# Kernel optimization log

Hardware: AMD Instinct MI355X
Metric: run time of the kernel (lower is better)

The kernel has to match this reference:

```python
import jax, jax.numpy as jnp
import numpy as np

N, CI, CO, K = 16384, 64, 64, 257


def setup_inputs() -> dict:
    key = jax.random.key(0)
    k1, k2 = jax.random.split(key)
    x = jax.random.normal(k1, (N, CI), dtype=jnp.float32)
    # lecun_normal-like scale over fan_in = K*CI
    kernel = jax.random.normal(k2, (K, CI, CO), dtype=jnp.float32) * (1.0 / np.sqrt(K * CI))
    bias = jnp.zeros((CO,), dtype=jnp.float32)
    return {"x": x, "kernel": kernel, "bias": bias}


def reference(x, kernel, bias):
    # Faithful translation of fconv1d.__call__ with strides=1, padding='valid'.
    Ci = x.shape[-1]
    Co = kernel.shape[-1]
    # h: (K, Ci*Co), flattened row-major so column j -> (ci=j//Co, co=j%Co)
    h = jnp.reshape(kernel, (kernel.shape[0], Ci * Co))
    # y: (N, Ci*Co), tiled so column j -> ci = j % Ci (exactly as jnp.tile does)
    y = jnp.tile(x, (1, Co))
    # Ci*Co independent 1D 'valid' convolutions (true convolution, kernel flipped)
    zflat = jax.vmap(lambda a, b: jnp.convolve(a, b, mode='valid'),
                     in_axes=-1, out_axes=-1)(y, h)  # (Nout, Ci*Co)
    # reduce over Ci exactly as the original reshape/sum does
    z = zflat.T.reshape((Co, Ci, -1)).sum(axis=1).T  # (Nout, Co)
    sps = 1  # strides = 1
    return z[::sps, :] + bias[None, :]
```

## Files before the change

### kernel.cpp

```cpp
#include <hip/hip_runtime.h>

#define NN   16384
#define CIN  64
#define COUT 64
#define KW   257
#define NOUT (NN - KW + 1)
#define BM   256
#define NKCH 8

typedef __attribute__((ext_vector_type(8))) short short8;
typedef __attribute__((ext_vector_type(8))) unsigned short ushortx8;
typedef __attribute__((ext_vector_type(4))) float floatx4;
typedef unsigned short ushort_t;

__device__ __forceinline__ ushort_t f2bf(float f) {
  union { float f; unsigned u; } c; c.f = f;
  unsigned u = c.u;
  return (ushort_t)((u + 0x7FFFu + ((u >> 16) & 1u)) >> 16);
}
__device__ __forceinline__ float bf2f(ushort_t h) {
  union { unsigned u; float f; } c; c.u = ((unsigned)h) << 16;
  return c.f;
}

__device__ __forceinline__ void cp16(const void* g, void* l) {
  auto gp = (const __attribute__((address_space(1))) unsigned int*)(unsigned long long)(uintptr_t)g;
  auto lp = (__attribute__((address_space(3))) unsigned int*)(unsigned int)(uintptr_t)l;
  __builtin_amdgcn_global_load_lds(gp, lp, 16, 0, 0);
}

__global__ void prep_convert(const float* __restrict__ x, const float* __restrict__ w,
                             ushort_t* __restrict__ xs, ushort_t* __restrict__ wsz) {
  const int c = blockIdx.x * blockDim.x + threadIdx.x;
  const float* src;
  ushort_t* dst;
  if (c < 131072) {
    const int row = c >> 3, ch = c & 7;
    src = x + (size_t)row * 64 + ((ch ^ (row & 7)) << 3);
    dst = xs + (size_t)row * 64 + (ch << 3);
  } else {
    const int c2 = c - 131072;
    const int t = c2 >> 9, r = (c2 >> 3) & 63, ch = c2 & 7;
    src = w + (size_t)(256 - t) * 4096 + r * 64 + ((ch ^ (r & 7)) << 3);
    dst = wsz + (size_t)t * 4096 + r * 64 + (ch << 3);
  }
  float4 v0 = *(const float4*)src;
  float4 v1 = *(const float4*)(src + 4);
  ushortx8 o;
  o[0] = f2bf(v0.x); o[1] = f2bf(v0.y); o[2] = f2bf(v0.z); o[3] = f2bf(v0.w);
  o[4] = f2bf(v1.x); o[5] = f2bf(v1.y); o[6] = f2bf(v1.z); o[7] = f2bf(v1.w);
  *(ushortx8*)dst = o;
}

__global__ __launch_bounds__(256, 2) void conv_gemm(
    const ushort_t* __restrict__ xs, const ushort_t* __restrict__ wsz,
    ushort_t* __restrict__ part) {
  __shared__ __align__(128) char smem[288 * 128 + 2 * 16384];
  char* Alds = smem;
  char* Wlds = smem + 288 * 128;

  const int tid  = threadIdx.x;
  const int lane = tid & 63;
  const int w    = tid >> 6;
  const int lr   = lane & 15;
  const int lh   = lane >> 4;

  const int mblk = blockIdx.x;
  const int g    = blockIdx.y;
  const int n0   = mblk * BM;
  const int t0   = (g * KW) / NKCH;
  const int t1   = ((g + 1) * KW) / NKCH;
  const int Tc   = t1 - t0;
  const int NCf  = Tc >> 1;
  const bool odd = Tc & 1;

  const ushort_t* agbase = xs + (size_t)(n0 + t0) * 64;
#pragma unroll
  for (int i = 0; i < 9; ++i)
    cp16(agbase + ((w * 9 + i) << 9) + lane * 8, Alds + ((w * 9 + i) << 10));

  const ushort_t* wgbase = wsz + (size_t)t0 * 4096;
#pragma unroll
  for (int s = 0; s < 2; ++s)
#pragma unroll
    for (int i = 0; i < 2; ++i)
      cp16(wgbase + (size_t)s * 4096 + ((w * 2 + i) << 9) + lane * 8,
           Wlds + s * 8192 + (w * 2 + i) * 1024);
  __syncthreads();

  floatx4 acc[4][4];
#pragma unroll
  for (int m = 0; m < 4; ++m)
#pragma unroll
    for (int nb = 0; nb < 4; ++nb)
      acc[m][nb] = (floatx4){0.f, 0.f, 0.f, 0.f};

  auto phase = [&](int ttL, int kk, const char* Wl) {
    short8 a[4], b[4];
#pragma unroll
    for (int m = 0; m < 4; ++m) {
      const int row = ttL + w * 64 + m * 16 + lr;
      a[m] = *(const short8*)(Alds + row * 128 + (((lh + 4 * kk) ^ (row & 7)) << 4));
    }
#pragma unroll
    for (int nb = 0; nb < 4; ++nb) {
      const int rw = nb * 16 + lr;
      b[nb] = *(const short8*)(Wl + rw * 128 + (((lh + 4 * kk) ^ (rw & 7)) << 4));
    }
    __builtin_amdgcn_s_barrier();
    asm volatile("s_waitcnt lgkmcnt(0)" ::: "memory");
    __builtin_amdgcn_sched_barrier(0);
    __builtin_amdgcn_s_setprio(1);
#pragma unroll
    for (int m = 0; m < 4; ++m)
#pragma unroll
      for (int nb = 0; nb < 4; ++nb)
        acc[m][nb] = __builtin_amdgcn_mfma_f32_16x16x32_bf16(a[m], b[nb], acc[m][nb], 0, 0, 0);
    __builtin_amdgcn_s_setprio(0);
    __builtin_amdgcn_s_barrier();
  };

  for (int cc = 0; cc < NCf; ++cc) {
    const int buf = cc & 1;
    if (cc + 1 < NCf) {
      const ushort_t* wg = wsz + (size_t)(t0 + (cc + 1) * 2) * 4096;
#pragma unroll
      for (int s = 0; s < 2; ++s)
#pragma unroll
        for (int i = 0; i < 2; ++i)
          cp16(wg + (size_t)s * 4096 + ((w * 2 + i) << 9) + lane * 8,
               Wlds + (buf ^ 1) * 16384 + s * 8192 + (w * 2 + i) * 1024);
      asm volatile("s_waitcnt vmcnt(4)" ::: "memory");
    } else if (odd) {
      const ushort_t* wg = wsz + (size_t)(t0 + NCf * 2) * 4096;
#pragma unroll
      for (int i = 0; i < 2; ++i)
        cp16(wg + ((w * 2 + i) << 9) + lane * 8,
             Wlds + (buf ^ 1) * 16384 + (w * 2 + i) * 1024);
      asm volatile("s_waitcnt vmcnt(2)" ::: "memory");
    } else {
      asm volatile("s_waitcnt vmcnt(0)" ::: "memory");
    }
    __builtin_amdgcn_s_barrier();

    const char* Wl = Wlds + buf * 16384;
    phase(cc * 2,     0, Wl);
    phase(cc * 2,     1, Wl);
    phase(cc * 2 + 1, 0, Wl + 8192);
    phase(cc * 2 + 1, 1, Wl + 8192);
  }
  if (odd) {
    asm volatile("s_waitcnt vmcnt(0)" ::: "memory");
    __builtin_amdgcn_s_barrier();
    const char* Wl = Wlds + (NCf & 1) * 16384;
    phase(Tc - 1, 0, Wl);
    phase(Tc - 1, 1, Wl);
  }

  ushort_t* pg = part + (size_t)g * (NOUT * 64);
#pragma unroll
  for (int m = 0; m < 4; ++m)
#pragma unroll
    for (int nb = 0; nb < 4; ++nb)
#pragma unroll
      for (int r = 0; r < 4; ++r) {
        const int row = n0 + w * 64 + m * 16 + lh * 4 + r;
        const int col = nb * 16 + lr;
        pg[(size_t)row * 64 + col] = f2bf(acc[m][nb][r]);
      }
}

__global__ void reduce_out(const ushort_t* __restrict__ part, const float* __restrict__ bias,
                           float* __restrict__ out) {
  const int i = blockIdx.x * blockDim.x + threadIdx.x;
  if (i >= NOUT * 8) return;
  const int colbase = (i & 7) * 8;
  float s[8];
#pragma unroll
  for (int j = 0; j < 8; ++j) s[j] = bias[colbase + j];
#pragma unroll
  for (int gg = 0; gg < NKCH; ++gg) {
    ushortx8 p = *(const ushortx8*)(part + (size_t)gg * (NOUT * 64) + (size_t)i * 8);
#pragma unroll
    for (int j = 0; j < 8; ++j) s[j] += bf2f(p[j]);
  }
  float4 o0 = {s[0], s[1], s[2], s[3]};
  float4 o1 = {s[4], s[5], s[6], s[7]};
  *(float4*)(out + (size_t)i * 8) = o0;
  *(float4*)(out + (size_t)i * 8 + 4) = o1;
}

__global__ void naive_conv(const float* __restrict__ x, const float* __restrict__ w,
                           const float* __restrict__ bias, float* __restrict__ out) {
  const int idx = blockIdx.x * blockDim.x + threadIdx.x;
  if (idx >= NOUT * COUT) return;
  const int n = idx / COUT, co = idx % COUT;
  float s = bias[co];
  for (int t = 0; t < KW; ++t) {
    const float* xr = x + (size_t)(n + t) * CIN;
    const float* wr = w + (size_t)(KW - 1 - t) * CIN * COUT + (size_t)co * CIN;
#pragma unroll 8
    for (int ci = 0; ci < CIN; ++ci) s += xr[ci] * wr[ci];
  }
  out[idx] = s;
}

extern "C" void kernel_launch(void* const* d_in, const int* in_sizes, int n_in,
                              void* d_out, int out_size, void* d_ws, size_t ws_size,
                              hipStream_t stream) {
  const float* x    = (const float*)d_in[0];
  const float* kern = (const float*)d_in[1];
  const float* bias = (const float*)d_in[2];
  float* out = (float*)d_out;

  const size_t xs_b   = (size_t)NN * CIN * 2;
  const size_t ws_b   = (size_t)KW * CIN * COUT * 2;
  const size_t part_b = (size_t)NKCH * NOUT * COUT * 2;
  const size_t need   = xs_b + ws_b + part_b;

  if (ws_size < need) {
    naive_conv<<<(NOUT * COUT + 255) / 256, 256, 0, stream>>>(x, kern, bias, out);
    return;
  }

  ushort_t* xs   = (ushort_t*)d_ws;
  ushort_t* wsz  = xs + (size_t)NN * CIN;
  ushort_t* part = wsz + (size_t)KW * CIN * COUT;

  prep_convert<<<1026, 256, 0, stream>>>(x, kern, xs, wsz);
  conv_gemm<<<dim3(NOUT / BM, NKCH), 256, 0, stream>>>(xs, wsz, part);
  reduce_out<<<(NOUT * 8 + 255) / 256, 256, 0, stream>>>(part, bias, out);
}
```

Baseline: 45.45 us.

## Double the M tile to 512 rows and pipeline weights one tap at a time

The conv GEMM block grows from 256 to 512 output rows with 512 threads, so each weight tap loaded into LDS is shared by twice as many rows. The old two-tap double buffer becomes a four-slot ring that prefetches one tap three steps ahead. The input is zero-padded so the last, partial tile can read past the end safely, and stores are masked for rows past the output length. The larger LDS footprint probably limits occupancy to one block per CU. Half of the last tile's compute is also wasted.

Result: slower. 47.84 us (+5.3%).

```diff
diff --git a/kernel.cpp b/kernel.cpp
--- a/kernel.cpp
+++ b/kernel.cpp
@@ -1,11 +1,12 @@
 #include <hip/hip_runtime.h>
 
 #define NN   16384
+#define NPAD 512
 #define CIN  64
 #define COUT 64
 #define KW   257
 #define NOUT (NN - KW + 1)
-#define BM   256
+#define BM   512
 #define NKCH 8
 
 typedef __attribute__((ext_vector_type(8))) short short8;
@@ -32,6 +33,12 @@
 __global__ void prep_convert(const float* __restrict__ x, const float* __restrict__ w,
                              ushort_t* __restrict__ xs, ushort_t* __restrict__ wsz) {
   const int c = blockIdx.x * blockDim.x + threadIdx.x;
+  if (c >= 262656) {
+    const int cz = c - 262656;
+    const int row = NN + (cz >> 3), ch = cz & 7;
+    *(ushortx8*)(xs + (size_t)row * 64 + (ch << 3)) = (ushortx8)(0);
+    return;
+  }
   const float* src;
   ushort_t* dst;
   if (c < 131072) {
@@ -52,12 +59,12 @@
   *(ushortx8*)dst = o;
 }
 
-__global__ __launch_bounds__(256, 2) void conv_gemm(
+__global__ __launch_bounds__(512, 2) void conv_gemm(
     const ushort_t* __restrict__ xs, const ushort_t* __restrict__ wsz,
     ushort_t* __restrict__ part) {
-  __shared__ __align__(128) char smem[288 * 128 + 2 * 16384];
+  __shared__ __align__(128) char smem[576 * 128 + 4 * 8192];
   char* Alds = smem;
-  char* Wlds = smem + 288 * 128;
+  char* Wlds = smem + 576 * 128;
 
   const int tid  = threadIdx.x;
   const int lane = tid & 63;
@@ -71,8 +78,6 @@
   const int t0   = (g * KW) / NKCH;
   const int t1   = ((g + 1) * KW) / NKCH;
   const int Tc   = t1 - t0;
-  const int NCf  = Tc >> 1;
-  const bool odd = Tc & 1;
 
   const ushort_t* agbase = xs + (size_t)(n0 + t0) * 64;
 #pragma unroll
@@ -81,12 +86,11 @@
 
   const ushort_t* wgbase = wsz + (size_t)t0 * 4096;
 #pragma unroll
-  for (int s = 0; s < 2; ++s)
-#pragma unroll
-    for (int i = 0; i < 2; ++i)
-      cp16(wgbase + (size_t)s * 4096 + ((w * 2 + i) << 9) + lane * 8,
-           Wlds + s * 8192 + (w * 2 + i) * 1024);
-  __syncthreads();
+  for (int t = 0; t < 3; ++t)
+    cp16(wgbase + (size_t)t * 4096 + (w << 9) + lane * 8,
+         Wlds + t * 8192 + (w << 10));
+  asm volatile("s_waitcnt vmcnt(2)" ::: "memory");
+  __builtin_amdgcn_s_barrier();
 
   floatx4 acc[4][4];
 #pragma unroll
@@ -95,66 +99,66 @@
     for (int nb = 0; nb < 4; ++nb)
       acc[m][nb] = (floatx4){0.f, 0.f, 0.f, 0.f};
 
-  auto phase = [&](int ttL, int kk, const char* Wl) {
-    short8 a[4], b[4];
-#pragma unroll
-    for (int m = 0; m < 4; ++m) {
-      const int row = ttL + w * 64 + m * 16 + lr;
-      a[m] = *(const short8*)(Alds + row * 128 + (((lh + 4 * kk) ^ (row & 7)) << 4));
+  for (int t = 0; t < Tc; ++t) {
+    const char* Wt = Wlds + (t & 3) * 8192;
+    {
+      short8 a[4], b[4];
+#pragma unroll
+      for (int m = 0; m < 4; ++m) {
+        const int row = t + w * 64 + m * 16 + lr;
+        a[m] = *(const short8*)(Alds + row * 128 + ((lh ^ (row & 7)) << 4));
+      }
+#pragma unroll
+      for (int nb = 0; nb < 4; ++nb) {
+        const int rw = nb * 16 + lr;
+        b[nb] = *(const short8*)(Wt + rw * 128 + ((lh ^ (rw & 7)) << 4));
+      }
+      if (t + 3 < Tc)
+        cp16(wsz + (size_t)(t0 + t + 3) * 4096 + (w << 9) + lane * 8,
+             Wlds + ((t + 3) & 3) * 8192 + (w << 10));
+      __builtin_amdgcn_s_barrier();
+      asm volatile("s_waitcnt lgkmcnt(0)" ::: "memory");
+      __builtin_amdgcn_sched_barrier(0);
+      __builtin_amdgcn_s_setprio(1);
+#pragma unroll
+      for (int m = 0; m < 4; ++m)
+#pragma unroll
+        for (int nb = 0; nb < 4; ++nb)
+          acc[m][nb] = __builtin_amdgcn_mfma_f32_16x16x32_bf16(a[m], b[nb], acc[m][nb], 0, 0, 0);
+      __builtin_amdgcn_s_setprio(0);
+      __builtin_amdgcn_s_barrier();
     }
-#pragma unroll
-    for (int nb = 0; nb < 4; ++nb) {
-      const int rw = nb * 16 + lr;
-      b[nb] = *(const short8*)(Wl + rw * 128 + (((lh + 4 * kk) ^ (rw & 7)) << 4));
+    {
+      short8 a[4], b[4];
+#pragma unroll
+      for (int m = 0; m < 4; ++m) {
+        const int row = t + w * 64 + m * 16 + lr;
+        a[m] = *(const short8*)(Alds + row * 128 + (((lh + 4) ^ (row & 7)) << 4));
+      }
+#pragma unroll
+      for (int nb = 0; nb < 4; ++nb) {
+        const int rw = nb * 16 + lr;
+        b[nb] = *(const short8*)(Wt + rw * 128 + (((lh + 4) ^ (rw & 7)) << 4));
+      }
+      __builtin_amdgcn_s_barrier();
+      asm volatile("s_waitcnt lgkmcnt(0)" ::: "memory");
+      __builtin_amdgcn_sched_barrier(0);
+      __builtin_amdgcn_s_setprio(1);
+#pragma unroll
+      for (int m = 0; m < 4; ++m)
+#pragma unroll
+        for (int nb = 0; nb < 4; ++nb)
+          acc[m][nb] = __builtin_amdgcn_mfma_f32_16x16x32_bf16(a[m], b[nb], acc[m][nb], 0, 0, 0);
+      __builtin_amdgcn_s_setprio(0);
+      if (t + 3 < Tc) {
+        asm volatile("s_waitcnt vmcnt(2)" ::: "memory");
+      } else if (t + 2 < Tc) {
+        asm volatile("s_waitcnt vmcnt(1)" ::: "memory");
+      } else if (t + 1 < Tc) {
+        asm volatile("s_waitcnt vmcnt(0)" ::: "memory");
+      }
+      __builtin_amdgcn_s_barrier();
     }
-    __builtin_amdgcn_s_barrier();
-    asm volatile("s_waitcnt lgkmcnt(0)" ::: "memory");
-    __builtin_amdgcn_sched_barrier(0);
-    __builtin_amdgcn_s_setprio(1);
-#pragma unroll
-    for (int m = 0; m < 4; ++m)
-#pragma unroll
-      for (int nb = 0; nb < 4; ++nb)
-        acc[m][nb] = __builtin_amdgcn_mfma_f32_16x16x32_bf16(a[m], b[nb], acc[m][nb], 0, 0, 0);
-    __builtin_amdgcn_s_setprio(0);
-    __builtin_amdgcn_s_barrier();
-  };
-
-  for (int cc = 0; cc < NCf; ++cc) {
-    const int buf = cc & 1;
-    if (cc + 1 < NCf) {
-      const ushort_t* wg = wsz + (size_t)(t0 + (cc + 1) * 2) * 4096;
-#pragma unroll
-      for (int s = 0; s < 2; ++s)
-#pragma unroll
-        for (int i = 0; i < 2; ++i)
-          cp16(wg + (size_t)s * 4096 + ((w * 2 + i) << 9) + lane * 8,
-               Wlds + (buf ^ 1) * 16384 + s * 8192 + (w * 2 + i) * 1024);
-      asm volatile("s_waitcnt vmcnt(4)" ::: "memory");
-    } else if (odd) {
-      const ushort_t* wg = wsz + (size_t)(t0 + NCf * 2) * 4096;
-#pragma unroll
-      for (int i = 0; i < 2; ++i)
-        cp16(wg + ((w * 2 + i) << 9) + lane * 8,
-             Wlds + (buf ^ 1) * 16384 + (w * 2 + i) * 1024);
-      asm volatile("s_waitcnt vmcnt(2)" ::: "memory");
-    } else {
-      asm volatile("s_waitcnt vmcnt(0)" ::: "memory");
-    }
-    __builtin_amdgcn_s_barrier();
-
-    const char* Wl = Wlds + buf * 16384;
-    phase(cc * 2,     0, Wl);
-    phase(cc * 2,     1, Wl);
-    phase(cc * 2 + 1, 0, Wl + 8192);
-    phase(cc * 2 + 1, 1, Wl + 8192);
-  }
-  if (odd) {
-    asm volatile("s_waitcnt vmcnt(0)" ::: "memory");
-    __builtin_amdgcn_s_barrier();
-    const char* Wl = Wlds + (NCf & 1) * 16384;
-    phase(Tc - 1, 0, Wl);
-    phase(Tc - 1, 1, Wl);
   }
 
   ushort_t* pg = part + (size_t)g * (NOUT * 64);
@@ -166,7 +170,7 @@
       for (int r = 0; r < 4; ++r) {
         const int row = n0 + w * 64 + m * 16 + lh * 4 + r;
         const int col = nb * 16 + lr;
-        pg[(size_t)row * 64 + col] = f2bf(acc[m][nb][r]);
+        if (row < NOUT) pg[(size_t)row * 64 + col] = f2bf(acc[m][nb][r]);
       }
 }
 
@@ -213,7 +217,7 @@
   const float* bias = (const float*)d_in[2];
   float* out = (float*)d_out;
 
-  const size_t xs_b   = (size_t)NN * CIN * 2;
+  const size_t xs_b   = (size_t)(NN + NPAD) * CIN * 2;
   const size_t ws_b   = (size_t)KW * CIN * COUT * 2;
   const size_t part_b = (size_t)NKCH * NOUT * COUT * 2;
   const size_t need   = xs_b + ws_b + part_b;
@@ -224,10 +228,10 @@
   }
 
   ushort_t* xs   = (ushort_t*)d_ws;
-  ushort_t* wsz  = xs + (size_t)NN * CIN;
+  ushort_t* wsz  = xs + (size_t)(NN + NPAD) * CIN;
   ushort_t* part = wsz + (size_t)KW * CIN * COUT;
 
-  prep_convert<<<1026, 256, 0, stream>>>(x, kern, xs, wsz);
-  conv_gemm<<<dim3(NOUT / BM, NKCH), 256, 0, stream>>>(xs, wsz, part);
+  prep_convert<<<1042, 256, 0, stream>>>(x, kern, xs, wsz);
+  conv_gemm<<<dim3(NOUT / BM + 1, NKCH), 512, 0, stream>>>(xs, wsz, part);
   reduce_out<<<(NOUT * 8 + 255) / 256, 256, 0, stream>>>(part, bias, out);
 }
```
